# Optimization experiments

Measured on AMD Instinct MI355X. Metric: run time of the kernel, lower is better.

## Reference

```python
import jax, jax.numpy as jnp
import numpy as np

D_MODEL = 1024
N_HEAD = 16
B, S = 2, 2048


def setup_inputs() -> dict:
    key = jax.random.key(0)
    ks = jax.random.split(key, 12)
    scale = 1.0 / np.sqrt(D_MODEL)
    inp = {
        "q": jax.random.normal(ks[0], (B, S, D_MODEL), jnp.float32),
        "k": jax.random.normal(ks[1], (B, S, D_MODEL), jnp.float32),
        "v": jax.random.normal(ks[2], (B, S, D_MODEL), jnp.float32),
        "mask": jax.random.randint(ks[3], (B, S, S), 0, 2, jnp.int32),
        "Wq": jax.random.normal(ks[4], (D_MODEL, D_MODEL), jnp.float32) * scale,
        "bq": jnp.zeros((D_MODEL,), jnp.float32),
        "Wk": jax.random.normal(ks[5], (D_MODEL, D_MODEL), jnp.float32) * scale,
        "bk": jnp.zeros((D_MODEL,), jnp.float32),
        "Wv": jax.random.normal(ks[6], (D_MODEL, D_MODEL), jnp.float32) * scale,
        "bv": jnp.zeros((D_MODEL,), jnp.float32),
        "Wo": jax.random.normal(ks[7], (D_MODEL, D_MODEL), jnp.float32) * scale,
        "bo": jnp.zeros((D_MODEL,), jnp.float32),
    }
    return inp


def reference(q, k, v, mask, Wq, bq, Wk, bk, Wv, bv, Wo, bo):
    b, s, d = q.shape
    dh = d // N_HEAD

    def proj_split(x, W, bias):
        # torch nn.Linear: x @ W.T + b; then split to [b, h, s, dh]
        y = x @ W.T + bias
        return y.reshape(b, s, N_HEAD, dh).transpose(0, 2, 1, 3)

    qh = proj_split(q, Wq, bq)
    kh = proj_split(k, Wk, bk)
    vh = proj_split(v, Wv, bv)

    # score: [b, h, s_q, s_k]
    score = jnp.einsum("bhqd,bhkd->bhqk", qh, kh) / jnp.sqrt(jnp.float32(dh))
    score = jnp.where(mask[:, None, :, :] == 0, jnp.float32(-10000.0), score)
    attn = jax.nn.softmax(score, axis=-1)

    out = jnp.einsum("bhqk,bhkd->bhqd", attn, vh)
    out = out.transpose(0, 2, 1, 3).reshape(b, s, d)
    return out @ Wo.T + bo
```

## Files before the change

kernel.cpp:

```cpp
#include <hip/hip_runtime.h>

typedef unsigned short u16;
typedef __bf16 bf16x8 __attribute__((ext_vector_type(8)));
typedef float f32x4 __attribute__((ext_vector_type(4)));

#define D_MODEL 1024
#define NH 16
#define DH 64
#define BB 2
#define SS 2048

#if __has_builtin(__builtin_amdgcn_exp2f)
#define EXP2f(x) __builtin_amdgcn_exp2f(x)
#else
#define EXP2f(x) exp2f(x)
#endif

__device__ __forceinline__ u16 f2bf_fast(float f) {
    union { float f; unsigned int u; } v; v.f = f;
    return (u16)((v.u + 0x8000u) >> 16);
}
__device__ __forceinline__ unsigned int cvtpk_bf16(float lo, float hi) {
    unsigned int r;
    asm("v_cvt_pk_bf16_f32 %0, %1, %2" : "=v"(r) : "v"(lo), "v"(hi));
    return r;
}
__device__ __forceinline__ uint4 pack8(const float4& a, const float4& b) {
    unsigned int a0 = __float_as_uint(a.x) + 0x8000u, a1 = __float_as_uint(a.y) + 0x8000u;
    unsigned int a2 = __float_as_uint(a.z) + 0x8000u, a3 = __float_as_uint(a.w) + 0x8000u;
    unsigned int b0 = __float_as_uint(b.x) + 0x8000u, b1 = __float_as_uint(b.y) + 0x8000u;
    unsigned int b2 = __float_as_uint(b.z) + 0x8000u, b3 = __float_as_uint(b.w) + 0x8000u;
    uint4 r;
    r.x = __builtin_amdgcn_perm(a1, a0, 0x07060302);
    r.y = __builtin_amdgcn_perm(a3, a2, 0x07060302);
    r.z = __builtin_amdgcn_perm(b1, b0, 0x07060302);
    r.w = __builtin_amdgcn_perm(b3, b2, 0x07060302);
    return r;
}

__device__ __forceinline__ void gld16(const void* g, void* l) {
    __builtin_amdgcn_global_load_lds(
        (const __attribute__((address_space(1))) unsigned int*)g,
        (__attribute__((address_space(3))) unsigned int*)l, 16, 0, 0);
}

__global__ __launch_bounds__(256) void prep_kernel(
    const float* __restrict__ Wq, const float* __restrict__ Wk,
    const float* __restrict__ Wv, const float* __restrict__ Wo, u16* __restrict__ cW,
    const float* __restrict__ q, const float* __restrict__ k,
    const float* __restrict__ v, u16* __restrict__ qb,
    const int* __restrict__ mask, unsigned long long* __restrict__ pm)
{
    int bid = blockIdx.x;
    if (bid < 2048) {
        int z = bid >> 9, x = bid & 511;
        const float* src = (z == 0) ? Wq : (z == 1) ? Wk : (z == 2) ? Wv : Wo;
        u16* dst = cW + (size_t)z * D_MODEL * D_MODEL;
        size_t base = ((size_t)x * 256 + threadIdx.x) * 8;
        float4 a = *reinterpret_cast<const float4*>(src + base);
        float4 b = *reinterpret_cast<const float4*>(src + base + 4);
        *reinterpret_cast<uint4*>(dst + base) = pack8(a, b);
    } else if (bid < 8192) {
        int x = bid - 2048;
        int z = x >> 11, xx = x & 2047;
        const float* src = (z == 0) ? q : (z == 1) ? k : v;
        u16* dst = qb + (size_t)z * BB * SS * D_MODEL;
        size_t base = ((size_t)xx * 256 + threadIdx.x) * 8;
        float4 a = *reinterpret_cast<const float4*>(src + base);
        float4 b = *reinterpret_cast<const float4*>(src + base + 4);
        *reinterpret_cast<uint4*>(dst + base) = pack8(a, b);
    } else {
        int x = bid - 8192;
        int gw = (x * 256 + threadIdx.x) >> 6;
        int l = threadIdx.x & 63;
#pragma unroll 4
        for (int i = 0; i < 32; ++i) {
            int widx = gw * 32 + i;
            int m = mask[(size_t)widx * 64 + l];
            unsigned long long bits = __ballot(m != 0);
            if (l == 0) pm[widx] = bits;
        }
    }
}

__device__ void gemm_qkv(const u16* __restrict__ A, const u16* __restrict__ W,
                         const float* __restrict__ bias, u16* __restrict__ outp,
                         float oscale)
{
    __shared__ __align__(16) u16 smem[128 * 144];
    u16* lA = smem;
    u16* lW = smem + 128 * 64;
    const int t = threadIdx.x, w = t >> 6, l = t & 63;
    const int blockM = blockIdx.x * 128, blockN = blockIdx.y * 128;
    const int lrow = l >> 3, lcol = (l & 7) * 8;
    const int quad = l >> 4, c16 = l & 15;

    f32x4 acc[4][4] = {};

    for (int kt = 0; kt < 16; ++kt) {
        __syncthreads();
#pragma unroll
        for (int i = 0; i < 4; ++i) {
            int c = w * 4 + i;
            int row = c * 8 + lrow;
            gld16(A + (size_t)(blockM + row) * 1024 + kt * 64 + lcol, &lA[c * 512]);
            gld16(W + (size_t)(blockN + row) * 1024 + kt * 64 + lcol, &lW[c * 512]);
        }
        __syncthreads();
#pragma unroll
        for (int ks = 0; ks < 2; ++ks) {
            bf16x8 af[4], bfr[4];
#pragma unroll
            for (int mi = 0; mi < 4; ++mi)
                af[mi] = *reinterpret_cast<const bf16x8*>(
                    &lA[((w & 1) * 64 + mi * 16 + c16) * 64 + ks * 32 + quad * 8]);
#pragma unroll
            for (int ni = 0; ni < 4; ++ni)
                bfr[ni] = *reinterpret_cast<const bf16x8*>(
                    &lW[((w >> 1) * 64 + ni * 16 + c16) * 64 + ks * 32 + quad * 8]);
#pragma unroll
            for (int mi = 0; mi < 4; ++mi)
#pragma unroll
                for (int ni = 0; ni < 4; ++ni)
                    acc[mi][ni] = __builtin_amdgcn_mfma_f32_16x16x32_bf16(
                        af[mi], bfr[ni], acc[mi][ni], 0, 0, 0);
        }
    }

    __syncthreads();
    const int m_base = (w & 1) * 64, n_base = (w >> 1) * 64;
#pragma unroll
    for (int ni = 0; ni < 4; ++ni) {
        int n_local = n_base + ni * 16 + c16;
        float bv = bias[blockN + n_local];
#pragma unroll
        for (int mi = 0; mi < 4; ++mi)
#pragma unroll
            for (int r = 0; r < 4; ++r) {
                int m_local = m_base + mi * 16 + quad * 4 + r;
                smem[m_local * 136 + n_local] =
                    f2bf_fast((acc[mi][ni][r] + bv) * oscale);
            }
    }
    __syncthreads();
    const int bb = blockM >> 11, s_base = blockM & 2047;
#pragma unroll
    for (int i = 0; i < 8; ++i) {
        int idx = t + i * 256;
        int mrow = idx >> 4, ch = idx & 15;
        uint4 val = *reinterpret_cast<const uint4*>(&smem[mrow * 136 + ch * 8]);
        int gn = blockN + ch * 8;
        int hh = gn >> 6, dh = gn & 63;
        *reinterpret_cast<uint4*>(
            outp + (((size_t)(bb * NH + hh)) * SS + s_base + mrow) * DH + dh) = val;
    }
}

__global__ __launch_bounds__(256) void qkv_kernel(
    const u16* __restrict__ qb, const u16* __restrict__ cW,
    const float* __restrict__ bq, const float* __restrict__ bk, const float* __restrict__ bv,
    u16* __restrict__ qh, u16* __restrict__ kh, u16* __restrict__ vh)
{
    int z = blockIdx.z;
    const u16* A = qb + (size_t)z * BB * SS * D_MODEL;
    const u16* W = cW + (size_t)z * D_MODEL * D_MODEL;
    const float* bias = (z == 0) ? bq : (z == 1) ? bk : bv;
    u16* out = (z == 0) ? qh : (z == 1) ? kh : vh;
    float oscale = (z == 0) ? 0.18033688011112042f : 1.0f;
    gemm_qkv(A, W, bias, out, oscale);
}

__global__ __launch_bounds__(256) void oproj_kernel(
    const u16* __restrict__ A, const u16* __restrict__ W,
    const float* __restrict__ bias, float* __restrict__ outp)
{
    __shared__ __align__(16) u16 lA[128 * 64];
    __shared__ __align__(16) u16 lW[64 * 64];
    const int t = threadIdx.x, w = t >> 6, l = t & 63;
    const int blockM = blockIdx.x * 128, blockN = blockIdx.y * 64;
    const int lrow = l >> 3, lcol = (l & 7) * 8;
    const int quad = l >> 4, c16 = l & 15;

    f32x4 acc[4][2] = {};

    for (int kt = 0; kt < 16; ++kt) {
        __syncthreads();
#pragma unroll
        for (int i = 0; i < 4; ++i) {
            int c = w * 4 + i;
            int row = c * 8 + lrow;
            gld16(A + (size_t)(blockM + row) * 1024 + kt * 64 + lcol, &lA[c * 512]);
        }
#pragma unroll
        for (int i = 0; i < 2; ++i) {
            int c = w * 2 + i;
            int row = c * 8 + lrow;
            gld16(W + (size_t)(blockN + row) * 1024 + kt * 64 + lcol, &lW[c * 512]);
        }
        __syncthreads();
#pragma unroll
        for (int ks = 0; ks < 2; ++ks) {
            bf16x8 af[4], bfr[2];
#pragma unroll
            for (int mi = 0; mi < 4; ++mi)
                af[mi] = *reinterpret_cast<const bf16x8*>(
                    &lA[((w & 1) * 64 + mi * 16 + c16) * 64 + ks * 32 + quad * 8]);
#pragma unroll
            for (int ni = 0; ni < 2; ++ni)
                bfr[ni] = *reinterpret_cast<const bf16x8*>(
                    &lW[((w >> 1) * 32 + ni * 16 + c16) * 64 + ks * 32 + quad * 8]);
#pragma unroll
            for (int mi = 0; mi < 4; ++mi)
#pragma unroll
                for (int ni = 0; ni < 2; ++ni)
                    acc[mi][ni] = __builtin_amdgcn_mfma_f32_16x16x32_bf16(
                        af[mi], bfr[ni], acc[mi][ni], 0, 0, 0);
        }
    }

    const int m0 = blockM + (w & 1) * 64, n0 = blockN + (w >> 1) * 32;
#pragma unroll
    for (int ni = 0; ni < 2; ++ni) {
        int n = n0 + ni * 16 + c16;
        float bv = bias[n];
#pragma unroll
        for (int mi = 0; mi < 4; ++mi) {
#pragma unroll
            for (int r = 0; r < 4; ++r) {
                int m = m0 + mi * 16 + quad * 4 + r;
                outp[(size_t)m * 1024 + n] = acc[mi][ni][r] + bv;
            }
        }
    }
}

__global__ __launch_bounds__(256, 2) void attn_kernel(
    const u16* __restrict__ qh, const u16* __restrict__ kh, const u16* __restrict__ vh,
    const unsigned long long* __restrict__ pm, u16* __restrict__ ao)
{
    __shared__ __align__(16) u16 lK[2][8 * 512];
    __shared__ __align__(16) u16 lVt[2][8 * 512];
    __shared__ __align__(16) u16 lP[128 * 72];

    const int t = threadIdx.x, w = t >> 6, l = t & 63;
    const int qt = blockIdx.x, h = blockIdx.y, b = blockIdx.z;
    const int sq0 = qt * 128;
    const size_t headbase = ((size_t)(b * NH + h)) * SS * DH;
    const int quad = l >> 4, c16 = l & 15;
    const int lrow = l >> 3, lcol = (l & 7) * 8;
    const int vd2 = t & 31, vg = t >> 5;

#pragma unroll
    for (int i = 0; i < 4; ++i) {
        int row = (w * 4 + i) * 8 + lrow;
        uint4 rq = *reinterpret_cast<const uint4*>(
            qh + headbase + (size_t)(sq0 + row) * DH + lcol);
        *reinterpret_cast<uint4*>(&lP[row * 72 + lcol]) = rq;
    }
    __asm__ volatile("s_waitcnt lgkmcnt(0)" ::: "memory");
    bf16x8 qf[2][2];
#pragma unroll
    for (int g = 0; g < 2; ++g)
#pragma unroll
        for (int ks = 0; ks < 2; ++ks)
            qf[g][ks] = *reinterpret_cast<const bf16x8*>(
                &lP[(w * 32 + g * 16 + c16) * 72 + ks * 32 + quad * 8]);

    f32x4 oAcc[2][4] = {};
    float rsumAcc[2] = {0.f, 0.f};
    const size_t pmrow0 = ((size_t)b * SS + sq0 + w * 32 + c16) * 32;
    const size_t pmrow1 = pmrow0 + 16 * 32;

    const int kcol = quad * 8;

    uint4 rk[2];
    unsigned int rvv[8];
    unsigned long long mw_cur0, mw_cur1, mw_next0, mw_next1;
#pragma unroll
    for (int i = 0; i < 2; ++i) {
        int c = w * 2 + i;
        rk[i] = *reinterpret_cast<const uint4*>(
            kh + headbase + (size_t)((c >> 1) * 16 + c16) * DH + (c & 1) * 32 + kcol);
    }
#pragma unroll
    for (int e = 0; e < 8; ++e)
        rvv[e] = *reinterpret_cast<const unsigned int*>(
            vh + headbase + (size_t)(vg * 8 + e) * DH + vd2 * 2);
    mw_cur0 = pm[pmrow0 + 0];
    mw_cur1 = pm[pmrow1 + 0];

    const int vchunk = (vd2 >> 3) * 2 + (vg >> 2);
    const int vlane = (vg & 3) * 16 + ((2 * vd2) & 15);

    for (int kt = 0; kt < 32; ++kt) {
        const int cur = kt & 1;
#pragma unroll
        for (int i = 0; i < 2; ++i)
            *reinterpret_cast<uint4*>(&lK[cur][(w * 2 + i) * 512 + l * 8]) = rk[i];
        {
            uint4 cA, cB;
            cA.x = __builtin_amdgcn_perm(rvv[1], rvv[0], 0x05040100);
            cA.y = __builtin_amdgcn_perm(rvv[3], rvv[2], 0x05040100);
            cA.z = __builtin_amdgcn_perm(rvv[5], rvv[4], 0x05040100);
            cA.w = __builtin_amdgcn_perm(rvv[7], rvv[6], 0x05040100);
            cB.x = __builtin_amdgcn_perm(rvv[1], rvv[0], 0x07060302);
            cB.y = __builtin_amdgcn_perm(rvv[3], rvv[2], 0x07060302);
            cB.z = __builtin_amdgcn_perm(rvv[5], rvv[4], 0x07060302);
            cB.w = __builtin_amdgcn_perm(rvv[7], rvv[6], 0x07060302);
            u16* vdst = &lVt[cur][vchunk * 512 + vlane * 8];
            *reinterpret_cast<uint4*>(vdst) = cA;
            *reinterpret_cast<uint4*>(vdst + 8) = cB;
        }
        __syncthreads();
        {
            int ktn = (kt < 31) ? kt + 1 : kt;
            const int sk0n = ktn * 64;
#pragma unroll
            for (int i = 0; i < 2; ++i) {
                int c = w * 2 + i;
                rk[i] = *reinterpret_cast<const uint4*>(
                    kh + headbase + (size_t)(sk0n + (c >> 1) * 16 + c16) * DH +
                    (c & 1) * 32 + kcol);
            }
#pragma unroll
            for (int e = 0; e < 8; ++e)
                rvv[e] = *reinterpret_cast<const unsigned int*>(
                    vh + headbase + (size_t)(sk0n + vg * 8 + e) * DH + vd2 * 2);
            mw_next0 = pm[pmrow0 + ktn];
            mw_next1 = pm[pmrow1 + ktn];
        }

        f32x4 sAcc[2][4] = {};
        __builtin_amdgcn_s_setprio(1);
#pragma unroll
        for (int ks = 0; ks < 2; ++ks) {
#pragma unroll
            for (int ni = 0; ni < 4; ++ni) {
                bf16x8 kf = *reinterpret_cast<const bf16x8*>(
                    &lK[cur][(ni * 2 + ks) * 512 + l * 8]);
                sAcc[0][ni] = __builtin_amdgcn_mfma_f32_16x16x32_bf16(
                    kf, qf[0][ks], sAcc[0][ni], 0, 0, 0);
                sAcc[1][ni] = __builtin_amdgcn_mfma_f32_16x16x32_bf16(
                    kf, qf[1][ks], sAcc[1][ni], 0, 0, 0);
            }
        }
        __builtin_amdgcn_s_setprio(0);

#pragma unroll
        for (int g = 0; g < 2; ++g) {
            unsigned long long mw = g ? mw_cur1 : mw_cur0;
            unsigned long long mq = mw >> (quad * 4);
            unsigned int mlo = (unsigned int)mq, mhi = (unsigned int)(mq >> 32);
            float rs = 0.f;
#pragma unroll
            for (int ni = 0; ni < 4; ++ni) {
                unsigned int half = (ni < 2) ? mlo : mhi;
                unsigned int sh = (ni & 1) * 16;
                float p0 = ((half >> (sh + 0)) & 1u) ? EXP2f(sAcc[g][ni][0]) : 0.f;
                float p1 = ((half >> (sh + 1)) & 1u) ? EXP2f(sAcc[g][ni][1]) : 0.f;
                float p2 = ((half >> (sh + 2)) & 1u) ? EXP2f(sAcc[g][ni][2]) : 0.f;
                float p3 = ((half >> (sh + 3)) & 1u) ? EXP2f(sAcc[g][ni][3]) : 0.f;
                rs += (p0 + p1) + (p2 + p3);
                uint2 pv;
                pv.x = cvtpk_bf16(p0, p1);
                pv.y = cvtpk_bf16(p2, p3);
                *reinterpret_cast<uint2*>(
                    &lP[(w * 32 + g * 16 + c16) * 72 + ni * 16 + quad * 4]) = pv;
            }
            if (g == 0) rsumAcc[0] += rs; else rsumAcc[1] += rs;
        }
        mw_cur0 = mw_next0; mw_cur1 = mw_next1;
        __asm__ volatile("s_waitcnt lgkmcnt(0)" ::: "memory");

        __builtin_amdgcn_s_setprio(1);
#pragma unroll
        for (int ks = 0; ks < 2; ++ks) {
            bf16x8 pf0 = *reinterpret_cast<const bf16x8*>(
                &lP[(w * 32 + c16) * 72 + ks * 32 + quad * 8]);
            bf16x8 pf1 = *reinterpret_cast<const bf16x8*>(
                &lP[(w * 32 + 16 + c16) * 72 + ks * 32 + quad * 8]);
#pragma unroll
            for (int no = 0; no < 4; ++no) {
                bf16x8 vf = *reinterpret_cast<const bf16x8*>(
                    &lVt[cur][(no * 2 + ks) * 512 + l * 8]);
                oAcc[0][no] = __builtin_amdgcn_mfma_f32_16x16x32_bf16(
                    pf0, vf, oAcc[0][no], 0, 0, 0);
                oAcc[1][no] = __builtin_amdgcn_mfma_f32_16x16x32_bf16(
                    pf1, vf, oAcc[1][no], 0, 0, 0);
            }
        }
        __builtin_amdgcn_s_setprio(0);
    }

    float linv[2][4];
#pragma unroll
    for (int g = 0; g < 2; ++g) {
        float s = (g == 0) ? rsumAcc[0] : rsumAcc[1];
        s += __shfl_xor(s, 16);
        s += __shfl_xor(s, 32);
        float rinv = 1.0f / s;
#pragma unroll
        for (int r = 0; r < 4; ++r)
            linv[g][r] = __shfl(rinv, quad * 4 + r);
    }
#pragma unroll
    for (int g = 0; g < 2; ++g)
#pragma unroll
        for (int no = 0; no < 4; ++no)
#pragma unroll
            for (int r = 0; r < 4; ++r)
                lP[(w * 32 + g * 16 + quad * 4 + r) * 72 + no * 16 + c16] =
                    f2bf_fast(oAcc[g][no][r] * linv[g][r]);
    __syncthreads();
#pragma unroll
    for (int i = 0; i < 4; ++i) {
        int idx = t + i * 256;
        int row = idx >> 3, ch = idx & 7;
        uint4 val = *reinterpret_cast<const uint4*>(&lP[row * 72 + ch * 8]);
        *reinterpret_cast<uint4*>(
            ao + ((size_t)b * SS + sq0 + row) * D_MODEL + h * DH + ch * 8) = val;
    }
}

extern "C" void kernel_launch(void* const* d_in, const int* in_sizes, int n_in,
                              void* d_out, int out_size, void* d_ws, size_t ws_size,
                              hipStream_t stream)
{
    const float* q    = (const float*)d_in[0];
    const float* k    = (const float*)d_in[1];
    const float* v    = (const float*)d_in[2];
    const int*   mask = (const int*)d_in[3];
    const float* Wq   = (const float*)d_in[4];
    const float* bq   = (const float*)d_in[5];
    const float* Wk   = (const float*)d_in[6];
    const float* bk   = (const float*)d_in[7];
    const float* Wv   = (const float*)d_in[8];
    const float* bv   = (const float*)d_in[9];
    const float* Wo   = (const float*)d_in[10];
    const float* bo   = (const float*)d_in[11];

    const size_t T4M = (size_t)BB * SS * D_MODEL;
    u16* qh = (u16*)d_ws;
    u16* kh = qh + T4M;
    u16* vh = kh + T4M;
    u16* ao = vh + T4M;
    u16* cW = ao + T4M;
    u16* qb = cW + 4 * (size_t)D_MODEL * D_MODEL;
    unsigned long long* pm = (unsigned long long*)(qb + 3 * T4M);
    float* out = (float*)d_out;

    prep_kernel<<<9216, 256, 0, stream>>>(Wq, Wk, Wv, Wo, cW, q, k, v, qb, mask, pm);
    qkv_kernel<<<dim3(32, 8, 3), 256, 0, stream>>>(qb, cW, bq, bk, bv, qh, kh, vh);
    attn_kernel<<<dim3(16, NH, BB), 256, 0, stream>>>(qh, kh, vh, pm, ao);
    oproj_kernel<<<dim3(32, 16), 256, 0, stream>>>(ao, cW + 3 * (size_t)D_MODEL * D_MODEL, bo, out);
}
```

Before: 295.4 us.

## Split attention KV range across two blocks and add combine kernel

Each attention block now processes half of the key sequence, doubling the grid from 512 to 1024 blocks. It writes unnormalized fp32 partial outputs and row sums to workspace, and a new combine kernel sums the two halves, normalizes, converts to bf16 and writes the head-interleaved output. The aim is better CU occupancy on a GPU with many CUs. The cost is extra global traffic for the fp32 partials (about 32MB written then read), plus one more kernel launch.

```diff
diff --git a/kernel.cpp b/kernel.cpp
--- a/kernel.cpp
+++ b/kernel.cpp
@@ -9,6 +9,8 @@
 #define DH 64
 #define BB 2
 #define SS 2048
+#define TOTROW (BB * NH * SS)
+#define TOTELEM ((size_t)TOTROW * DH)
 
 #if __has_builtin(__builtin_amdgcn_exp2f)
 #define EXP2f(x) __builtin_amdgcn_exp2f(x)
@@ -236,19 +238,23 @@
 
 __global__ __launch_bounds__(256, 2) void attn_kernel(
     const u16* __restrict__ qh, const u16* __restrict__ kh, const u16* __restrict__ vh,
-    const unsigned long long* __restrict__ pm, u16* __restrict__ ao)
+    const unsigned long long* __restrict__ pm,
+    float* __restrict__ pO, float* __restrict__ prs)
 {
     __shared__ __align__(16) u16 lK[2][8 * 512];
     __shared__ __align__(16) u16 lVt[2][8 * 512];
     __shared__ __align__(16) u16 lP[128 * 72];
 
     const int t = threadIdx.x, w = t >> 6, l = t & 63;
-    const int qt = blockIdx.x, h = blockIdx.y, b = blockIdx.z;
+    const int qt = blockIdx.x;
+    const int h = blockIdx.y >> 1, half = blockIdx.y & 1;
+    const int b = blockIdx.z;
     const int sq0 = qt * 128;
     const size_t headbase = ((size_t)(b * NH + h)) * SS * DH;
     const int quad = l >> 4, c16 = l & 15;
     const int lrow = l >> 3, lcol = (l & 7) * 8;
     const int vd2 = t & 31, vg = t >> 5;
+    const int kt0 = half * 16, ktE = kt0 + 16;
 
 #pragma unroll
     for (int i = 0; i < 4; ++i) {
@@ -276,23 +282,24 @@
     uint4 rk[2];
     unsigned int rvv[8];
     unsigned long long mw_cur0, mw_cur1, mw_next0, mw_next1;
+    const int sk00 = kt0 * 64;
 #pragma unroll
     for (int i = 0; i < 2; ++i) {
         int c = w * 2 + i;
         rk[i] = *reinterpret_cast<const uint4*>(
-            kh + headbase + (size_t)((c >> 1) * 16 + c16) * DH + (c & 1) * 32 + kcol);
+            kh + headbase + (size_t)(sk00 + (c >> 1) * 16 + c16) * DH + (c & 1) * 32 + kcol);
     }
 #pragma unroll
     for (int e = 0; e < 8; ++e)
         rvv[e] = *reinterpret_cast<const unsigned int*>(
-            vh + headbase + (size_t)(vg * 8 + e) * DH + vd2 * 2);
-    mw_cur0 = pm[pmrow0 + 0];
-    mw_cur1 = pm[pmrow1 + 0];
+            vh + headbase + (size_t)(sk00 + vg * 8 + e) * DH + vd2 * 2);
+    mw_cur0 = pm[pmrow0 + kt0];
+    mw_cur1 = pm[pmrow1 + kt0];
 
     const int vchunk = (vd2 >> 3) * 2 + (vg >> 2);
     const int vlane = (vg & 3) * 16 + ((2 * vd2) & 15);
 
-    for (int kt = 0; kt < 32; ++kt) {
+    for (int kt = kt0; kt < ktE; ++kt) {
         const int cur = kt & 1;
 #pragma unroll
         for (int i = 0; i < 2; ++i)
@@ -313,7 +320,7 @@
         }
         __syncthreads();
         {
-            int ktn = (kt < 31) ? kt + 1 : kt;
+            int ktn = (kt < ktE - 1) ? kt + 1 : kt;
             const int sk0n = ktn * 64;
 #pragma unroll
             for (int i = 0; i < 2; ++i) {
@@ -354,12 +361,12 @@
             float rs = 0.f;
 #pragma unroll
             for (int ni = 0; ni < 4; ++ni) {
-                unsigned int half = (ni < 2) ? mlo : mhi;
+                unsigned int half_m = (ni < 2) ? mlo : mhi;
                 unsigned int sh = (ni & 1) * 16;
-                float p0 = ((half >> (sh + 0)) & 1u) ? EXP2f(sAcc[g][ni][0]) : 0.f;
-                float p1 = ((half >> (sh + 1)) & 1u) ? EXP2f(sAcc[g][ni][1]) : 0.f;
-                float p2 = ((half >> (sh + 2)) & 1u) ? EXP2f(sAcc[g][ni][2]) : 0.f;
-                float p3 = ((half >> (sh + 3)) & 1u) ? EXP2f(sAcc[g][ni][3]) : 0.f;
+                float p0 = ((half_m >> (sh + 0)) & 1u) ? EXP2f(sAcc[g][ni][0]) : 0.f;
+                float p1 = ((half_m >> (sh + 1)) & 1u) ? EXP2f(sAcc[g][ni][1]) : 0.f;
+                float p2 = ((half_m >> (sh + 2)) & 1u) ? EXP2f(sAcc[g][ni][2]) : 0.f;
+                float p3 = ((half_m >> (sh + 3)) & 1u) ? EXP2f(sAcc[g][ni][3]) : 0.f;
                 rs += (p0 + p1) + (p2 + p3);
                 uint2 pv;
                 pv.x = cvtpk_bf16(p0, p1);
@@ -392,34 +399,52 @@
         __builtin_amdgcn_s_setprio(0);
     }
 
-    float linv[2][4];
+    const size_t pbase = ((size_t)(half * BB + b) * NH + h) * SS + sq0;
+    float* pOrow = pO + pbase * DH;
 #pragma unroll
     for (int g = 0; g < 2; ++g) {
-        float s = (g == 0) ? rsumAcc[0] : rsumAcc[1];
+        float s = rsumAcc[g];
         s += __shfl_xor(s, 16);
         s += __shfl_xor(s, 32);
-        float rinv = 1.0f / s;
-#pragma unroll
-        for (int r = 0; r < 4; ++r)
-            linv[g][r] = __shfl(rinv, quad * 4 + r);
-    }
-#pragma unroll
-    for (int g = 0; g < 2; ++g)
+        if (quad == 0)
+            prs[pbase + w * 32 + g * 16 + c16] = s;
 #pragma unroll
         for (int no = 0; no < 4; ++no)
 #pragma unroll
-            for (int r = 0; r < 4; ++r)
-                lP[(w * 32 + g * 16 + quad * 4 + r) * 72 + no * 16 + c16] =
-                    f2bf_fast(oAcc[g][no][r] * linv[g][r]);
-    __syncthreads();
-#pragma unroll
-    for (int i = 0; i < 4; ++i) {
-        int idx = t + i * 256;
-        int row = idx >> 3, ch = idx & 7;
-        uint4 val = *reinterpret_cast<const uint4*>(&lP[row * 72 + ch * 8]);
-        *reinterpret_cast<uint4*>(
-            ao + ((size_t)b * SS + sq0 + row) * D_MODEL + h * DH + ch * 8) = val;
-    }
+            for (int r = 0; r < 4; ++r) {
+                int m_local = w * 32 + g * 16 + quad * 4 + r;
+                pOrow[(size_t)m_local * DH + no * 16 + c16] = oAcc[g][no][r];
+            }
+    }
+}
+
+__global__ __launch_bounds__(256) void combine_kernel(
+    const float* __restrict__ pO, const float* __restrict__ prs, u16* __restrict__ ao)
+{
+    int gid = blockIdx.x * 256 + threadIdx.x;
+    if ((size_t)gid >= TOTELEM / 8) return;
+    size_t e0 = (size_t)gid * 8;
+    int row = gid >> 3;
+    int col = (gid & 7) * 8;
+    float inv = 1.0f / (prs[row] + prs[TOTROW + row]);
+    const float* p0 = pO + e0;
+    const float* p1 = pO + TOTELEM + e0;
+    float4 a0 = *reinterpret_cast<const float4*>(p0);
+    float4 a1 = *reinterpret_cast<const float4*>(p0 + 4);
+    float4 b0 = *reinterpret_cast<const float4*>(p1);
+    float4 b1 = *reinterpret_cast<const float4*>(p1 + 4);
+    float4 s0, s1;
+    s0.x = (a0.x + b0.x) * inv; s0.y = (a0.y + b0.y) * inv;
+    s0.z = (a0.z + b0.z) * inv; s0.w = (a0.w + b0.w) * inv;
+    s1.x = (a1.x + b1.x) * inv; s1.y = (a1.y + b1.y) * inv;
+    s1.z = (a1.z + b1.z) * inv; s1.w = (a1.w + b1.w) * inv;
+    uint4 vpk = pack8(s0, s1);
+    int b = row / (NH * SS);
+    int hs = row - b * NH * SS;
+    int h = hs >> 11;
+    int s = hs & (SS - 1);
+    *reinterpret_cast<uint4*>(
+        ao + ((size_t)b * SS + s) * D_MODEL + h * DH + col) = vpk;
 }
 
 extern "C" void kernel_launch(void* const* d_in, const int* in_sizes, int n_in,
@@ -447,10 +472,13 @@
     u16* cW = ao + T4M;
     u16* qb = cW + 4 * (size_t)D_MODEL * D_MODEL;
     unsigned long long* pm = (unsigned long long*)(qb + 3 * T4M);
+    float* pO = (float*)(pm + (size_t)BB * SS * 32);
+    float* prs = pO + 2 * TOTELEM;
     float* out = (float*)d_out;
 
     prep_kernel<<<9216, 256, 0, stream>>>(Wq, Wk, Wv, Wo, cW, q, k, v, qb, mask, pm);
     qkv_kernel<<<dim3(32, 8, 3), 256, 0, stream>>>(qb, cW, bq, bk, bv, qh, kh, vh);
-    attn_kernel<<<dim3(16, NH, BB), 256, 0, stream>>>(qh, kh, vh, pm, ao);
+    attn_kernel<<<dim3(16, NH * 2, BB), 256, 0, stream>>>(qh, kh, vh, pm, pO, prs);
+    combine_kernel<<<2048, 256, 0, stream>>>(pO, prs, ao);
     oproj_kernel<<<dim3(32, 16), 256, 0, stream>>>(ao, cW + 3 * (size_t)D_MODEL * D_MODEL, bo, out);
 }
```

Measured after the change: 308.6 us. +4.5%, slower.
